# Optimization experiments

Hardware: AMD Instinct MI355X
Metric: run time of the kernel (lower is better)

Reference implementation:

```python
import jax, jax.numpy as jnp
import numpy as np

B, N, C = 2, 2048, 1024
H, D = 16, 64          # num_heads, head_dim
FF = 4096              # mlp hidden = 4*C
EPS = 1e-5


def layernorm(x, g, b):
    mu = jnp.mean(x, axis=-1, keepdims=True)
    var = jnp.mean((x - mu) ** 2, axis=-1, keepdims=True)
    return (x - mu) * jax.lax.rsqrt(var + EPS) * g + b


def setup_inputs() -> dict:
    key = jax.random.key(0)
    ks = jax.random.split(key, 8)
    s = lambda d: 1.0 / np.sqrt(d)
    return {
        "x": jax.random.normal(ks[0], (B, N, C), jnp.float32),
        "ln1_g": jnp.ones((C,), jnp.float32),
        "ln1_b": jnp.zeros((C,), jnp.float32),
        "qkv_w": jax.random.normal(ks[1], (3 * C, C), jnp.float32) * s(C),
        "proj_w": jax.random.normal(ks[2], (C, C), jnp.float32) * s(C),
        "proj_b": jnp.zeros((C,), jnp.float32),
        "ln2_g": jnp.ones((C,), jnp.float32),
        "ln2_b": jnp.zeros((C,), jnp.float32),
        "w1": jax.random.normal(ks[3], (FF, C), jnp.float32) * s(C),
        "b1": jnp.zeros((FF,), jnp.float32),
        "w2": jax.random.normal(ks[4], (C, FF), jnp.float32) * s(FF),
        "b2": jnp.zeros((C,), jnp.float32),
    }


def reference(x, ln1_g, ln1_b, qkv_w, proj_w, proj_b, ln2_g, ln2_b, w1, b1, w2, b2):
    # ---- attention sub-block ----
    h = layernorm(x, ln1_g, ln1_b)                       # [B,N,C]
    qkv = h @ qkv_w.T                                    # [B,N,3C]
    qkv = qkv.reshape(B, N, 3, H, D).transpose(2, 0, 3, 1, 4)  # [3,B,H,N,D]
    q, k, v = qkv[0], qkv[1], qkv[2]
    scale = D ** -0.5
    attn = jnp.einsum("bhnd,bhmd->bhnm", q, k) * scale   # [B,H,N,N]
    attn = jax.nn.softmax(attn, axis=-1)
    ao = jnp.einsum("bhnm,bhmd->bhnd", attn, v)          # [B,H,N,D]
    ao = ao.transpose(0, 2, 1, 3).reshape(B, N, C)
    x = x + ao @ proj_w.T + proj_b
    # ---- MLP sub-block ----
    h2 = layernorm(x, ln2_g, ln2_b)
    mlp = jax.nn.gelu(h2 @ w1.T + b1, approximate=False) @ w2.T + b2
    return x + mlp
```

## Files before the change

### kernel.cpp

```cpp
#include <hip/hip_runtime.h>
#include <hip/hip_bf16.h>

typedef __hip_bfloat16 obf;
typedef __attribute__((ext_vector_type(8))) __bf16 bf16x8;
typedef __attribute__((ext_vector_type(4))) float f32x4;

#define DEVINL __device__ __forceinline__

DEVINL void gload_lds16(const void* g, void* l) {
  __builtin_amdgcn_global_load_lds((const __attribute__((address_space(1))) void*)g,
                                   (__attribute__((address_space(3))) void*)l,
                                   16, 0, 0);
}

__global__ void __launch_bounds__(256) f2b_kernel(const float* __restrict__ in,
                                                  __bf16* __restrict__ out, int n8)
{
  const int i = blockIdx.x * 256 + threadIdx.x;
  if (i >= n8) return;
  const float4 a = ((const float4*)in)[i * 2];
  const float4 b = ((const float4*)in)[i * 2 + 1];
  bf16x8 o;
  o[0] = (__bf16)a.x; o[1] = (__bf16)a.y; o[2] = (__bf16)a.z; o[3] = (__bf16)a.w;
  o[4] = (__bf16)b.x; o[5] = (__bf16)b.y; o[6] = (__bf16)b.z; o[7] = (__bf16)b.w;
  ((bf16x8*)out)[i] = o;
}

__global__ void __launch_bounds__(256) ln_kernel(const float* __restrict__ xin,
    const float* __restrict__ g, const float* __restrict__ b, obf* __restrict__ out)
{
  const int row = blockIdx.x;
  const int t = threadIdx.x;
  const int lane = t & 63, w = t >> 6;
  float4 f = ((const float4*)xin)[(size_t)row * 256 + t];
  float v[4] = { f.x, f.y, f.z, f.w };
  float s1 = v[0] + v[1] + v[2] + v[3];
  float s2 = v[0]*v[0] + v[1]*v[1] + v[2]*v[2] + v[3]*v[3];
  #pragma unroll
  for (int off = 32; off >= 1; off >>= 1) {
    s1 += __shfl_xor(s1, off);
    s2 += __shfl_xor(s2, off);
  }
  __shared__ float red[8];
  if (lane == 0) { red[w] = s1; red[4 + w] = s2; }
  __syncthreads();
  s1 = red[0] + red[1] + red[2] + red[3];
  s2 = red[4] + red[5] + red[6] + red[7];
  const float mu = s1 * (1.f / 1024.f);
  const float var = s2 * (1.f / 1024.f) - mu * mu;
  const float rs = rsqrtf(var + 1e-5f);
  const float4 gv = ((const float4*)g)[t];
  const float4 bv = ((const float4*)b)[t];
  obf* op = out + (size_t)row * 1024 + t * 4;
  op[0] = __float2bfloat16((v[0] - mu) * rs * gv.x + bv.x);
  op[1] = __float2bfloat16((v[1] - mu) * rs * gv.y + bv.y);
  op[2] = __float2bfloat16((v[2] - mu) * rs * gv.z + bv.z);
  op[3] = __float2bfloat16((v[3] - mu) * rs * gv.w + bv.w);
}

enum { EPI_NONE = 0, EPI_BIAS_RES_F32OUT = 1, EPI_BIAS_GELU = 2, EPI_BIAS_RESF32_F32OUT = 3 };

template<int EPI, int NI>
__global__ void __launch_bounds__(256, 2) gemm_bt(
    const obf* __restrict__ A, const obf* __restrict__ Bw,
    void* __restrict__ Cout, const float* __restrict__ bias,
    const void* __restrict__ resid, int M, int N, int K)
{
  __shared__ __align__(16) char As[128 * 64 * 2];
  __shared__ __align__(16) char Bs[NI * 32 * 64 * 2];
  const int tid = threadIdx.x;
  const int lane = tid & 63;
  const int w = tid >> 6, wr = w >> 1, wc = w & 1;
  const int bm = blockIdx.y * 128, bn = blockIdx.x * (NI * 32);
  const size_t lda = (size_t)K * 2;

  f32x4 acc[4][NI];
  #pragma unroll
  for (int i = 0; i < 4; i++)
    #pragma unroll
    for (int j = 0; j < NI; j++) {
      acc[i][j][0] = 0.f; acc[i][j][1] = 0.f; acc[i][j][2] = 0.f; acc[i][j][3] = 0.f;
    }

  for (int k0 = 0; k0 < K; k0 += 64) {
    #pragma unroll
    for (int i = 0; i < 4; i++) {
      const int ci = tid + 256 * i;
      const int r = ci >> 3;
      const int gb = ((ci & 7) * 16) ^ ((r & 7) << 4);
      gload_lds16((const char*)A + (size_t)(bm + r) * lda + (size_t)k0 * 2 + gb, As + ci * 16);
    }
    #pragma unroll
    for (int i = 0; i < NI; i++) {
      const int ci = tid + 256 * i;
      const int r = ci >> 3;
      const int gb = ((ci & 7) * 16) ^ ((r & 7) << 4);
      gload_lds16((const char*)Bw + (size_t)(bn + r) * lda + (size_t)k0 * 2 + gb, Bs + ci * 16);
    }
    __syncthreads();

    bf16x8 af[4][2], bfr[NI][2];
    #pragma unroll
    for (int mi = 0; mi < 4; mi++) {
      const int r = wr * 64 + mi * 16 + (lane & 15);
      #pragma unroll
      for (int ks = 0; ks < 2; ks++) {
        const int cb = ks * 64 + ((lane >> 4) * 16);
        af[mi][ks] = *(const bf16x8*)(As + r * 128 + (cb ^ ((r & 7) << 4)));
      }
    }
    #pragma unroll
    for (int ni = 0; ni < NI; ni++) {
      const int r = wc * (NI * 16) + ni * 16 + (lane & 15);
      #pragma unroll
      for (int ks = 0; ks < 2; ks++) {
        const int cb = ks * 64 + ((lane >> 4) * 16);
        bfr[ni][ks] = *(const bf16x8*)(Bs + r * 128 + (cb ^ ((r & 7) << 4)));
      }
    }
    #pragma unroll
    for (int ks = 0; ks < 2; ks++)
      #pragma unroll
      for (int mi = 0; mi < 4; mi++)
        #pragma unroll
        for (int ni = 0; ni < NI; ni++)
          acc[mi][ni] = __builtin_amdgcn_mfma_f32_16x16x32_bf16(af[mi][ks], bfr[ni][ks], acc[mi][ni], 0, 0, 0);
    __syncthreads();
  }

  #pragma unroll
  for (int mi = 0; mi < 4; mi++) {
    #pragma unroll
    for (int ni = 0; ni < NI; ni++) {
      const int col = bn + wc * (NI * 16) + ni * 16 + (lane & 15);
      float bv = 0.f;
      if (EPI != EPI_NONE) bv = bias[col];
      #pragma unroll
      for (int r = 0; r < 4; r++) {
        const int row = bm + wr * 64 + mi * 16 + ((lane >> 4) << 2) + r;
        const float vacc = acc[mi][ni][r];
        const size_t idx = (size_t)row * N + col;
        if (EPI == EPI_NONE) {
          ((obf*)Cout)[idx] = __float2bfloat16(vacc);
        } else if (EPI == EPI_BIAS_RES_F32OUT) {
          const float x0 = ((const float*)resid)[idx];
          ((float*)Cout)[idx] = vacc + bv + x0;
        } else if (EPI == EPI_BIAS_GELU) {
          const float u = vacc + bv;
          ((obf*)Cout)[idx] = __float2bfloat16(0.5f * u * (1.f + erff(u * 0.70710678118f)));
        } else {
          const float x0 = ((const float*)resid)[idx];
          ((float*)Cout)[idx] = vacc + bv + x0;
        }
      }
    }
  }
}

__global__ void __launch_bounds__(256) vtrans_kernel(const obf* __restrict__ qkv, obf* __restrict__ vt)
{
  const int bh = blockIdx.y;
  const int b = bh >> 4, h = bh & 15;
  const int n0 = blockIdx.x * 64;
  __shared__ __bf16 tile[64][72];
  const int t = threadIdx.x;
  {
    const int n = t >> 2;
    const int c0 = (t & 3) * 16;
    const __bf16* src = (const __bf16*)qkv + ((size_t)(b * 2048 + n0 + n)) * 3072 + 2048 + h * 64 + c0;
    bf16x8 u0 = *(const bf16x8*)src;
    bf16x8 u1 = *(const bf16x8*)(src + 8);
    #pragma unroll
    for (int j = 0; j < 8; j++) { tile[n][c0 + j] = u0[j]; tile[n][c0 + 8 + j] = u1[j]; }
  }
  __syncthreads();
  {
    const int d = t >> 2;
    const int c0 = (t & 3) * 16;
    bf16x8 o0, o1;
    #pragma unroll
    for (int j = 0; j < 8; j++) { o0[j] = tile[c0 + j][d]; o1[j] = tile[c0 + 8 + j][d]; }
    __bf16* dst = (__bf16*)vt + ((size_t)bh * 64 + d) * 2048 + n0 + c0;
    *(bf16x8*)dst = o0;
    *(bf16x8*)(dst + 8) = o1;
  }
}

__global__ void __launch_bounds__(256, 2) attn_kernel(
    const obf* __restrict__ qkv_, const obf* __restrict__ vt_, obf* __restrict__ ao)
{
  const __bf16* qkv = (const __bf16*)qkv_;
  const __bf16* vt  = (const __bf16*)vt_;
  const int bid = blockIdx.x;
  const int xcd = bid & 7, idx = bid >> 3;
  const int bh = xcd * 4 + (idx >> 4);
  const int q0 = (idx & 15) * 128;
  const int b = bh >> 4, h = bh & 15;
  const int tid = threadIdx.x, lane = tid & 63, w = tid >> 6;
  const int l15 = lane & 15, hi = lane >> 4;

  __shared__ __align__(16) char Ks[64 * 128];
  __shared__ __align__(16) char Vs[64 * 128];
  __shared__ __align__(16) char Ps[4 * 32 * 128];

  bf16x8 qf[2][2];
  #pragma unroll
  for (int mi = 0; mi < 2; mi++) {
    const int qrow = q0 + w * 32 + mi * 16 + l15;
    #pragma unroll
    for (int ks = 0; ks < 2; ks++)
      qf[mi][ks] = *(const bf16x8*)(qkv + ((size_t)(b * 2048 + qrow)) * 3072 + h * 64 + ks * 32 + hi * 8);
  }

  f32x4 o[2][4];
  #pragma unroll
  for (int i = 0; i < 2; i++)
    #pragma unroll
    for (int j = 0; j < 4; j++) { o[i][j][0]=0.f; o[i][j][1]=0.f; o[i][j][2]=0.f; o[i][j][3]=0.f; }
  float lrow[8];
  #pragma unroll
  for (int i = 0; i < 8; i++) lrow[i] = 0.f;

  const float kfac = 0.125f * 1.44269504089f;

  bf16x8 pk[2], pv[2];
  #pragma unroll
  for (int i = 0; i < 2; i++) {
    const int ci = tid + 256 * i;
    const int kr = ci >> 3, kc = (ci & 7) * 8;
    pk[i] = *(const bf16x8*)(qkv + ((size_t)(b * 2048 + kr)) * 3072 + 1024 + h * 64 + kc);
    pv[i] = *(const bf16x8*)(vt + ((size_t)bh * 64 + kr) * 2048 + kc);
  }
  #pragma unroll
  for (int i = 0; i < 2; i++) {
    const int ci = tid + 256 * i;
    const int kr = ci >> 3, kcb = (ci & 7) * 16;
    *(bf16x8*)(Ks + kr * 128 + (kcb ^ ((kr & 7) << 4))) = pk[i];
    *(bf16x8*)(Vs + kr * 128 + (kcb ^ ((kr & 7) << 4))) = pv[i];
  }
  __syncthreads();

  for (int kt = 0; kt < 2048; kt += 64) {
    if (kt + 64 < 2048) {
      #pragma unroll
      for (int i = 0; i < 2; i++) {
        const int ci = tid + 256 * i;
        const int kr = ci >> 3, kc = (ci & 7) * 8;
        pk[i] = *(const bf16x8*)(qkv + ((size_t)(b * 2048 + kt + 64 + kr)) * 3072 + 1024 + h * 64 + kc);
        pv[i] = *(const bf16x8*)(vt + ((size_t)bh * 64 + kr) * 2048 + kt + 64 + kc);
      }
    }

    f32x4 s[2][4];
    #pragma unroll
    for (int i = 0; i < 2; i++)
      #pragma unroll
      for (int j = 0; j < 4; j++) { s[i][j][0]=0.f; s[i][j][1]=0.f; s[i][j][2]=0.f; s[i][j][3]=0.f; }
    #pragma unroll
    for (int ni = 0; ni < 4; ni++) {
      const int r = ni * 16 + l15;
      const bf16x8 kf0 = *(const bf16x8*)(Ks + r * 128 + ((hi * 16) ^ ((r & 7) << 4)));
      const bf16x8 kf1 = *(const bf16x8*)(Ks + r * 128 + ((64 + hi * 16) ^ ((r & 7) << 4)));
      #pragma unroll
      for (int mi = 0; mi < 2; mi++) {
        s[mi][ni] = __builtin_amdgcn_mfma_f32_16x16x32_bf16(qf[mi][0], kf0, s[mi][ni], 0, 0, 0);
        s[mi][ni] = __builtin_amdgcn_mfma_f32_16x16x32_bf16(qf[mi][1], kf1, s[mi][ni], 0, 0, 0);
      }
    }

    #pragma unroll
    for (int mi = 0; mi < 2; mi++) {
      #pragma unroll
      for (int r = 0; r < 4; r++) {
        const int ri = mi * 4 + r;
        const int qrl = mi * 16 + (hi << 2) + r;
        char* psrow = Ps + w * 4096 + qrl * 128;
        float psum = 0.f;
        #pragma unroll
        for (int ni = 0; ni < 4; ni++) {
          const float p = exp2f(s[mi][ni][r] * kfac);
          psum += p;
          *(__bf16*)(psrow + (((ni * 16 + l15) * 2) ^ ((qrl & 7) << 4))) = (__bf16)p;
        }
        lrow[ri] += psum;
      }
    }

    #pragma unroll
    for (int ks = 0; ks < 2; ks++) {
      bf16x8 pa[2];
      #pragma unroll
      for (int mi = 0; mi < 2; mi++) {
        const int rr = mi * 16 + l15;
        pa[mi] = *(const bf16x8*)(Ps + w * 4096 + rr * 128 + (((ks * 32 + hi * 8) * 2) ^ ((rr & 7) << 4)));
      }
      #pragma unroll
      for (int df = 0; df < 4; df++) {
        const int dr = df * 16 + l15;
        const int cb = (ks * 32 + hi * 8) * 2;
        const bf16x8 vb = *(const bf16x8*)(Vs + dr * 128 + (cb ^ ((dr & 7) << 4)));
        #pragma unroll
        for (int mi = 0; mi < 2; mi++)
          o[mi][df] = __builtin_amdgcn_mfma_f32_16x16x32_bf16(pa[mi], vb, o[mi][df], 0, 0, 0);
      }
    }

    __syncthreads();
    if (kt + 64 < 2048) {
      #pragma unroll
      for (int i = 0; i < 2; i++) {
        const int ci = tid + 256 * i;
        const int kr = ci >> 3, kcb = (ci & 7) * 16;
        *(bf16x8*)(Ks + kr * 128 + (kcb ^ ((kr & 7) << 4))) = pk[i];
        *(bf16x8*)(Vs + kr * 128 + (kcb ^ ((kr & 7) << 4))) = pv[i];
      }
    }
    __syncthreads();
  }

  #pragma unroll
  for (int ri = 0; ri < 8; ri++) {
    lrow[ri] += __shfl_xor(lrow[ri], 1);
    lrow[ri] += __shfl_xor(lrow[ri], 2);
    lrow[ri] += __shfl_xor(lrow[ri], 4);
    lrow[ri] += __shfl_xor(lrow[ri], 8);
  }
  #pragma unroll
  for (int mi = 0; mi < 2; mi++) {
    #pragma unroll
    for (int r = 0; r < 4; r++) {
      const float inv = 1.f / lrow[mi * 4 + r];
      const int qrow = q0 + w * 32 + mi * 16 + (hi << 2) + r;
      #pragma unroll
      for (int df = 0; df < 4; df++) {
        const int col = h * 64 + df * 16 + l15;
        ao[((size_t)(b * 2048 + qrow)) * 1024 + col] = __float2bfloat16(o[mi][df][r] * inv);
      }
    }
  }
}

extern "C" void kernel_launch(void* const* d_in, const int* in_sizes, int n_in,
                              void* d_out, int out_size, void* d_ws, size_t ws_size,
                              hipStream_t stream) {
  const float* x      = (const float*)d_in[0];
  const float* ln1_g  = (const float*)d_in[1];
  const float* ln1_b  = (const float*)d_in[2];
  const float* qkv_w  = (const float*)d_in[3];
  const float* proj_w = (const float*)d_in[4];
  const float* proj_b = (const float*)d_in[5];
  const float* ln2_g  = (const float*)d_in[6];
  const float* ln2_b  = (const float*)d_in[7];
  const float* w1     = (const float*)d_in[8];
  const float* b1     = (const float*)d_in[9];
  const float* w2     = (const float*)d_in[10];
  const float* b2     = (const float*)d_in[11];
  float* out = (float*)d_out;

  char* ws = (char*)d_ws;
  float* x2   = (float*)ws;
  obf*   h    = (obf*)(ws + (16u << 20));
  obf*   qkv  = (obf*)(ws + (24u << 20));
  obf*   ao   = (obf*)(ws + (48u << 20));
  obf*   m1   = (obf*)(ws + (24u << 20));
  __bf16* slot = (__bf16*)(ws + (56u << 20));
  __bf16* wb_w2 = (__bf16*)(ws + (16u << 20));

  const int M = 4096;

  f2b_kernel<<<(3072 * 1024 / 8 + 255) / 256, 256, 0, stream>>>(qkv_w, slot, 3072 * 1024 / 8);
  ln_kernel<<<M, 256, 0, stream>>>(x, ln1_g, ln1_b, h);
  gemm_bt<EPI_NONE, 4><<<dim3(3072 / 128, M / 128), 256, 0, stream>>>(
      h, (const obf*)slot, qkv, nullptr, nullptr, M, 3072, 1024);
  vtrans_kernel<<<dim3(32, 32), 256, 0, stream>>>(qkv, (obf*)slot);
  attn_kernel<<<512, 256, 0, stream>>>(qkv, (const obf*)slot, ao);
  f2b_kernel<<<(1024 * 1024 / 8 + 255) / 256, 256, 0, stream>>>(proj_w, slot, 1024 * 1024 / 8);
  gemm_bt<EPI_BIAS_RES_F32OUT, 2><<<dim3(1024 / 64, M / 128), 256, 0, stream>>>(
      ao, (const obf*)slot, x2, proj_b, x, M, 1024, 1024);
  ln_kernel<<<M, 256, 0, stream>>>(x2, ln2_g, ln2_b, h);
  f2b_kernel<<<(4096 * 1024 / 8 + 255) / 256, 256, 0, stream>>>(w1, slot, 4096 * 1024 / 8);
  gemm_bt<EPI_BIAS_GELU, 4><<<dim3(4096 / 128, M / 128), 256, 0, stream>>>(
      h, (const obf*)slot, m1, b1, nullptr, M, 4096, 1024);
  f2b_kernel<<<(4096 * 1024 / 8 + 255) / 256, 256, 0, stream>>>(w2, wb_w2, 4096 * 1024 / 8);
  gemm_bt<EPI_BIAS_RESF32_F32OUT, 2><<<dim3(1024 / 64, M / 128), 256, 0, stream>>>(
      m1, (const obf*)wb_w2, out, b2, x2, M, 1024, 4096);
}
```

Measured before the change: 259.6 us.

## Split attention work across eight waves of sixteen query rows each

The attention kernel now launches 512 threads per block. Each of 8 wavefronts handles 16 query rows instead of 4 wavefronts handling 32 rows. This lowers per-wave register use for accumulators and scores, and raises the number of waves available to hide LDS and global latency. K/V tile loading is spread over twice as many threads. The cost is that each K/V fragment read from LDS now feeds only one MFMA row-block, so LDS reads per MFMA roughly double.

```diff
diff --git a/kernel.cpp b/kernel.cpp
--- a/kernel.cpp
+++ b/kernel.cpp
@@ -186,7 +186,7 @@
   }
 }
 
-__global__ void __launch_bounds__(256, 2) attn_kernel(
+__global__ void __launch_bounds__(512, 2) attn_kernel(
     const obf* __restrict__ qkv_, const obf* __restrict__ vt_, obf* __restrict__ ao)
 {
   const __bf16* qkv = (const __bf16*)qkv_;
@@ -201,141 +201,106 @@
 
   __shared__ __align__(16) char Ks[64 * 128];
   __shared__ __align__(16) char Vs[64 * 128];
-  __shared__ __align__(16) char Ps[4 * 32 * 128];
-
-  bf16x8 qf[2][2];
-  #pragma unroll
-  for (int mi = 0; mi < 2; mi++) {
-    const int qrow = q0 + w * 32 + mi * 16 + l15;
+  __shared__ __align__(16) char Ps[8 * 16 * 128];
+
+  bf16x8 qf[2];
+  {
+    const int qrow = q0 + w * 16 + l15;
     #pragma unroll
     for (int ks = 0; ks < 2; ks++)
-      qf[mi][ks] = *(const bf16x8*)(qkv + ((size_t)(b * 2048 + qrow)) * 3072 + h * 64 + ks * 32 + hi * 8);
-  }
-
-  f32x4 o[2][4];
-  #pragma unroll
-  for (int i = 0; i < 2; i++)
-    #pragma unroll
-    for (int j = 0; j < 4; j++) { o[i][j][0]=0.f; o[i][j][1]=0.f; o[i][j][2]=0.f; o[i][j][3]=0.f; }
-  float lrow[8];
-  #pragma unroll
-  for (int i = 0; i < 8; i++) lrow[i] = 0.f;
+      qf[ks] = *(const bf16x8*)(qkv + ((size_t)(b * 2048 + qrow)) * 3072 + h * 64 + ks * 32 + hi * 8);
+  }
+
+  f32x4 o[4];
+  #pragma unroll
+  for (int j = 0; j < 4; j++) { o[j][0]=0.f; o[j][1]=0.f; o[j][2]=0.f; o[j][3]=0.f; }
+  float lrow[4] = { 0.f, 0.f, 0.f, 0.f };
 
   const float kfac = 0.125f * 1.44269504089f;
 
-  bf16x8 pk[2], pv[2];
-  #pragma unroll
-  for (int i = 0; i < 2; i++) {
-    const int ci = tid + 256 * i;
-    const int kr = ci >> 3, kc = (ci & 7) * 8;
-    pk[i] = *(const bf16x8*)(qkv + ((size_t)(b * 2048 + kr)) * 3072 + 1024 + h * 64 + kc);
-    pv[i] = *(const bf16x8*)(vt + ((size_t)bh * 64 + kr) * 2048 + kc);
-  }
-  #pragma unroll
-  for (int i = 0; i < 2; i++) {
-    const int ci = tid + 256 * i;
-    const int kr = ci >> 3, kcb = (ci & 7) * 16;
-    *(bf16x8*)(Ks + kr * 128 + (kcb ^ ((kr & 7) << 4))) = pk[i];
-    *(bf16x8*)(Vs + kr * 128 + (kcb ^ ((kr & 7) << 4))) = pv[i];
+  bf16x8 pk, pv;
+  {
+    const int kr = tid >> 3, kc = (tid & 7) * 8;
+    pk = *(const bf16x8*)(qkv + ((size_t)(b * 2048 + kr)) * 3072 + 1024 + h * 64 + kc);
+    pv = *(const bf16x8*)(vt + ((size_t)bh * 64 + kr) * 2048 + kc);
+  }
+  {
+    const int kr = tid >> 3, kcb = (tid & 7) * 16;
+    *(bf16x8*)(Ks + kr * 128 + (kcb ^ ((kr & 7) << 4))) = pk;
+    *(bf16x8*)(Vs + kr * 128 + (kcb ^ ((kr & 7) << 4))) = pv;
   }
   __syncthreads();
 
   for (int kt = 0; kt < 2048; kt += 64) {
     if (kt + 64 < 2048) {
-      #pragma unroll
-      for (int i = 0; i < 2; i++) {
-        const int ci = tid + 256 * i;
-        const int kr = ci >> 3, kc = (ci & 7) * 8;
-        pk[i] = *(const bf16x8*)(qkv + ((size_t)(b * 2048 + kt + 64 + kr)) * 3072 + 1024 + h * 64 + kc);
-        pv[i] = *(const bf16x8*)(vt + ((size_t)bh * 64 + kr) * 2048 + kt + 64 + kc);
-      }
-    }
-
-    f32x4 s[2][4];
-    #pragma unroll
-    for (int i = 0; i < 2; i++)
-      #pragma unroll
-      for (int j = 0; j < 4; j++) { s[i][j][0]=0.f; s[i][j][1]=0.f; s[i][j][2]=0.f; s[i][j][3]=0.f; }
+      const int kr = tid >> 3, kc = (tid & 7) * 8;
+      pk = *(const bf16x8*)(qkv + ((size_t)(b * 2048 + kt + 64 + kr)) * 3072 + 1024 + h * 64 + kc);
+      pv = *(const bf16x8*)(vt + ((size_t)bh * 64 + kr) * 2048 + kt + 64 + kc);
+    }
+
+    f32x4 s[4];
+    #pragma unroll
+    for (int j = 0; j < 4; j++) { s[j][0]=0.f; s[j][1]=0.f; s[j][2]=0.f; s[j][3]=0.f; }
     #pragma unroll
     for (int ni = 0; ni < 4; ni++) {
       const int r = ni * 16 + l15;
       const bf16x8 kf0 = *(const bf16x8*)(Ks + r * 128 + ((hi * 16) ^ ((r & 7) << 4)));
       const bf16x8 kf1 = *(const bf16x8*)(Ks + r * 128 + ((64 + hi * 16) ^ ((r & 7) << 4)));
-      #pragma unroll
-      for (int mi = 0; mi < 2; mi++) {
-        s[mi][ni] = __builtin_amdgcn_mfma_f32_16x16x32_bf16(qf[mi][0], kf0, s[mi][ni], 0, 0, 0);
-        s[mi][ni] = __builtin_amdgcn_mfma_f32_16x16x32_bf16(qf[mi][1], kf1, s[mi][ni], 0, 0, 0);
-      }
-    }
-
-    #pragma unroll
-    for (int mi = 0; mi < 2; mi++) {
-      #pragma unroll
-      for (int r = 0; r < 4; r++) {
-        const int ri = mi * 4 + r;
-        const int qrl = mi * 16 + (hi << 2) + r;
-        char* psrow = Ps + w * 4096 + qrl * 128;
-        float psum = 0.f;
-        #pragma unroll
-        for (int ni = 0; ni < 4; ni++) {
-          const float p = exp2f(s[mi][ni][r] * kfac);
-          psum += p;
-          *(__bf16*)(psrow + (((ni * 16 + l15) * 2) ^ ((qrl & 7) << 4))) = (__bf16)p;
-        }
-        lrow[ri] += psum;
-      }
+      s[ni] = __builtin_amdgcn_mfma_f32_16x16x32_bf16(qf[0], kf0, s[ni], 0, 0, 0);
+      s[ni] = __builtin_amdgcn_mfma_f32_16x16x32_bf16(qf[1], kf1, s[ni], 0, 0, 0);
+    }
+
+    #pragma unroll
+    for (int r = 0; r < 4; r++) {
+      const int qrl = (hi << 2) + r;
+      char* psrow = Ps + w * 2048 + qrl * 128;
+      float psum = 0.f;
+      #pragma unroll
+      for (int ni = 0; ni < 4; ni++) {
+        const float p = exp2f(s[ni][r] * kfac);
+        psum += p;
+        *(__bf16*)(psrow + (((ni * 16 + l15) * 2) ^ ((qrl & 7) << 4))) = (__bf16)p;
+      }
+      lrow[r] += psum;
     }
 
     #pragma unroll
     for (int ks = 0; ks < 2; ks++) {
-      bf16x8 pa[2];
-      #pragma unroll
-      for (int mi = 0; mi < 2; mi++) {
-        const int rr = mi * 16 + l15;
-        pa[mi] = *(const bf16x8*)(Ps + w * 4096 + rr * 128 + (((ks * 32 + hi * 8) * 2) ^ ((rr & 7) << 4)));
-      }
+      const int rr = l15;
+      const bf16x8 pa = *(const bf16x8*)(Ps + w * 2048 + rr * 128 + (((ks * 32 + hi * 8) * 2) ^ ((rr & 7) << 4)));
       #pragma unroll
       for (int df = 0; df < 4; df++) {
         const int dr = df * 16 + l15;
         const int cb = (ks * 32 + hi * 8) * 2;
         const bf16x8 vb = *(const bf16x8*)(Vs + dr * 128 + (cb ^ ((dr & 7) << 4)));
-        #pragma unroll
-        for (int mi = 0; mi < 2; mi++)
-          o[mi][df] = __builtin_amdgcn_mfma_f32_16x16x32_bf16(pa[mi], vb, o[mi][df], 0, 0, 0);
+        o[df] = __builtin_amdgcn_mfma_f32_16x16x32_bf16(pa, vb, o[df], 0, 0, 0);
       }
     }
 
     __syncthreads();
     if (kt + 64 < 2048) {
-      #pragma unroll
-      for (int i = 0; i < 2; i++) {
-        const int ci = tid + 256 * i;
-        const int kr = ci >> 3, kcb = (ci & 7) * 16;
-        *(bf16x8*)(Ks + kr * 128 + (kcb ^ ((kr & 7) << 4))) = pk[i];
-        *(bf16x8*)(Vs + kr * 128 + (kcb ^ ((kr & 7) << 4))) = pv[i];
-      }
+      const int kr = tid >> 3, kcb = (tid & 7) * 16;
+      *(bf16x8*)(Ks + kr * 128 + (kcb ^ ((kr & 7) << 4))) = pk;
+      *(bf16x8*)(Vs + kr * 128 + (kcb ^ ((kr & 7) << 4))) = pv;
     }
     __syncthreads();
   }
 
   #pragma unroll
-  for (int ri = 0; ri < 8; ri++) {
-    lrow[ri] += __shfl_xor(lrow[ri], 1);
-    lrow[ri] += __shfl_xor(lrow[ri], 2);
-    lrow[ri] += __shfl_xor(lrow[ri], 4);
-    lrow[ri] += __shfl_xor(lrow[ri], 8);
-  }
-  #pragma unroll
-  for (int mi = 0; mi < 2; mi++) {
-    #pragma unroll
-    for (int r = 0; r < 4; r++) {
-      const float inv = 1.f / lrow[mi * 4 + r];
-      const int qrow = q0 + w * 32 + mi * 16 + (hi << 2) + r;
-      #pragma unroll
-      for (int df = 0; df < 4; df++) {
-        const int col = h * 64 + df * 16 + l15;
-        ao[((size_t)(b * 2048 + qrow)) * 1024 + col] = __float2bfloat16(o[mi][df][r] * inv);
-      }
+  for (int r = 0; r < 4; r++) {
+    lrow[r] += __shfl_xor(lrow[r], 1);
+    lrow[r] += __shfl_xor(lrow[r], 2);
+    lrow[r] += __shfl_xor(lrow[r], 4);
+    lrow[r] += __shfl_xor(lrow[r], 8);
+  }
+  #pragma unroll
+  for (int r = 0; r < 4; r++) {
+    const float inv = 1.f / lrow[r];
+    const int qrow = q0 + w * 16 + (hi << 2) + r;
+    #pragma unroll
+    for (int df = 0; df < 4; df++) {
+      const int col = h * 64 + df * 16 + l15;
+      ao[((size_t)(b * 2048 + qrow)) * 1024 + col] = __float2bfloat16(o[df][r] * inv);
     }
   }
 }
@@ -373,7 +338,7 @@
   gemm_bt<EPI_NONE, 4><<<dim3(3072 / 128, M / 128), 256, 0, stream>>>(
       h, (const obf*)slot, qkv, nullptr, nullptr, M, 3072, 1024);
   vtrans_kernel<<<dim3(32, 32), 256, 0, stream>>>(qkv, (obf*)slot);
-  attn_kernel<<<512, 256, 0, stream>>>(qkv, (const obf*)slot, ao);
+  attn_kernel<<<512, 512, 0, stream>>>(qkv, (const obf*)slot, ao);
   f2b_kernel<<<(1024 * 1024 / 8 + 255) / 256, 256, 0, stream>>>(proj_w, slot, 1024 * 1024 / 8);
   gemm_bt<EPI_BIAS_RES_F32OUT, 2><<<dim3(1024 / 64, M / 128), 256, 0, stream>>>(
       ao, (const obf*)slot, x2, proj_b, x, M, 1024, 1024);
```

After: 252.3 us. 2.8% less time.
